# Kernel optimization log

Hardware: AMD Instinct MI355X
Metric: run time of the kernel (lower is better)

The kernel has to match this reference:

```python
import jax, jax.numpy as jnp
import numpy as np

NUM_GROUPS = 4194304  # 2^22 groups
GROUP_SIZE = 32
PACKED_GROUP_SIZE = GROUP_SIZE // 2 + 1  # 16 data bytes + 1 scale byte


def setup_inputs() -> dict:
    key = jax.random.key(0)
    packed = jax.random.randint(key, (NUM_GROUPS * PACKED_GROUP_SIZE,), 0, 256, dtype=jnp.int32)
    return {"packed": packed, "group_size": GROUP_SIZE, "ebits": 2, "mbits": 1}


def reference(packed, group_size, ebits, mbits):
    # MX4 -> fp32 dequantization: unpack 4-bit nibbles + per-group exp2 scale.
    packed_group_size = group_size // 2 + 1
    num_groups = packed.shape[0] // packed_group_size
    clamp_max = 2 ** (2 ** ebits - 1)                      # 8 for ebits=2
    max_val = clamp_max * (2.0 - 2.0 ** (-mbits))          # 12.0 for mbits=1

    pg = packed.reshape(num_groups, packed_group_size)
    # last byte of each group is the shared scale exponent (biased by 127)
    log_scale = jnp.clip(pg[:, -1].astype(jnp.float32) - 127.0, -126.0, 127.0)
    group_scale = jnp.exp2(log_scale)                      # (num_groups,)

    data = pg[:, : group_size // 2]                        # (num_groups, group_size//2)
    low = (data & 15).astype(jnp.float32)
    high = ((data >> 4) & 15).astype(jnp.float32)
    # interleave low/high nibbles: element order [low0, high0, low1, high1, ...]
    unpacked = jnp.stack([low, high], axis=-1).reshape(num_groups, group_size)
    unpacked = unpacked - jnp.float32(clamp_max)

    out = unpacked / jnp.float32(max_val) * group_scale[:, None]
    return out.reshape(-1).astype(jnp.float32)
```

## Files before the change

### kernel.cpp

```cpp
#include <hip/hip_runtime.h>


constexpr int kGroupSize = 32;
constexpr int kPGS = kGroupSize / 2 + 1;

__global__ __launch_bounds__(256) void dequant_mxfp4_kernel(
    const int* __restrict__ packed,
    const int* __restrict__ ebits_p,
    const int* __restrict__ mbits_p,
    float* __restrict__ out,
    int n_vec4)
{
    int tid = blockIdx.x * 256 + threadIdx.x;
    if (tid >= n_vec4) return;

    int ebits = ebits_p[0];
    int mbits = mbits_p[0];
    float clamp_max = (float)(1 << ((1 << ebits) - 1));
    float inv_max   = 1.0f / (clamp_max * (2.0f - exp2f((float)(-mbits))));

    int g  = tid >> 3;
    int b0 = (tid & 7) * 2;
    int base = g * kPGS;

    int w0 = packed[base + b0];
    int w1 = packed[base + b0 + 1];
    int s  = packed[base + kGroupSize / 2];

    int e = s - 127;
    e = min(max(e, -126), 127);
    float coef = ldexpf(1.0f, e) * inv_max;

    float4 r;
    r.x = ((float)(w0 & 15)        - clamp_max) * coef;
    r.y = ((float)((w0 >> 4) & 15) - clamp_max) * coef;
    r.z = ((float)(w1 & 15)        - clamp_max) * coef;
    r.w = ((float)((w1 >> 4) & 15) - clamp_max) * coef;

    reinterpret_cast<float4*>(out)[tid] = r;
}

extern "C" void kernel_launch(void* const* d_in, const int* in_sizes, int n_in,
                              void* d_out, int out_size, void* d_ws, size_t ws_size,
                              hipStream_t stream) {
    const int* packed  = (const int*)d_in[0];
    const int* ebits_p = (const int*)d_in[2];
    const int* mbits_p = (const int*)d_in[3];
    float* out = (float*)d_out;

    int n_vec4 = out_size / 4;
    int grid = (n_vec4 + 255) / 256;
    dequant_mxfp4_kernel<<<grid, 256, 0, stream>>>(packed, ebits_p, mbits_p, out, n_vec4);
}
```

Before: 690.6 us.

## Stage packed groups in LDS with vectorized loads, process 128 groups per block

Each block now cooperatively copies 128 packed groups into shared memory using 16-byte vector loads, then each thread dequantizes four float4 outputs from LDS. This replaces per-thread unaligned scalar global loads, including the redundant scale reads, with coalesced wide loads. It adds a block-wide barrier and shared-memory traffic. Scale computation is also folded into a single ldexpf.

```diff
diff --git a/kernel.cpp b/kernel.cpp
--- a/kernel.cpp
+++ b/kernel.cpp
@@ -1,43 +1,65 @@
 #include <hip/hip_runtime.h>
 
 
-constexpr int kGroupSize = 32;
-constexpr int kPGS = kGroupSize / 2 + 1;
+constexpr int kPGS = 17;
+constexpr int kGroupsPerBlock = 128;
+constexpr int kWordsPerBlock = kGroupsPerBlock * kPGS;
+constexpr int kVec4PerBlock  = kGroupsPerBlock * 8;
 
 __global__ __launch_bounds__(256) void dequant_mxfp4_kernel(
     const int* __restrict__ packed,
     const int* __restrict__ ebits_p,
     const int* __restrict__ mbits_p,
     float* __restrict__ out,
-    int n_vec4)
+    int num_groups)
 {
-    int tid = blockIdx.x * 256 + threadIdx.x;
-    if (tid >= n_vec4) return;
+    __shared__ int lds[kWordsPerBlock];
 
-    int ebits = ebits_p[0];
-    int mbits = mbits_p[0];
-    float clamp_max = (float)(1 << ((1 << ebits) - 1));
-    float inv_max   = 1.0f / (clamp_max * (2.0f - exp2f((float)(-mbits))));
+    const int block_g0 = blockIdx.x * kGroupsPerBlock;
+    const int groups_here = min(kGroupsPerBlock, num_groups - block_g0);
+    const int words = groups_here * kPGS;
+    const int* src = packed + (size_t)block_g0 * kPGS;
 
-    int g  = tid >> 3;
-    int b0 = (tid & 7) * 2;
-    int base = g * kPGS;
+    if (words == kWordsPerBlock) {
+        const int4* __restrict__ src4 = (const int4*)src;
+        int4* lds4 = (int4*)lds;
+        #pragma unroll
+        for (int i = threadIdx.x; i < kWordsPerBlock / 4; i += 256)
+            lds4[i] = src4[i];
+    } else {
+        for (int i = threadIdx.x; i < words; i += 256)
+            lds[i] = src[i];
+    }
+    __syncthreads();
 
-    int w0 = packed[base + b0];
-    int w1 = packed[base + b0 + 1];
-    int s  = packed[base + kGroupSize / 2];
+    const int ebits = ebits_p[0];
+    const int mbits = mbits_p[0];
+    const float clamp_max = (float)(1 << ((1 << ebits) - 1));
+    const float inv_max   = 1.0f / (clamp_max * (2.0f - exp2f((float)(-mbits))));
 
-    int e = s - 127;
-    e = min(max(e, -126), 127);
-    float coef = ldexpf(1.0f, e) * inv_max;
+    float4* __restrict__ dst = (float4*)out + (size_t)blockIdx.x * kVec4PerBlock;
+    const int nv = groups_here * 8;
 
-    float4 r;
-    r.x = ((float)(w0 & 15)        - clamp_max) * coef;
-    r.y = ((float)((w0 >> 4) & 15) - clamp_max) * coef;
-    r.z = ((float)(w1 & 15)        - clamp_max) * coef;
-    r.w = ((float)((w1 >> 4) & 15) - clamp_max) * coef;
+    #pragma unroll
+    for (int it = 0; it < 4; ++it) {
+        int v = it * 256 + (int)threadIdx.x;
+        if (v >= nv) break;
+        int g = v >> 3;
+        int j = (v & 7) * 2;
+        int w0 = lds[g * kPGS + j];
+        int w1 = lds[g * kPGS + j + 1];
+        int s  = lds[g * kPGS + 16];
 
-    reinterpret_cast<float4*>(out)[tid] = r;
+        int e = min(max(s - 127, -126), 127);
+        float coef = ldexpf(inv_max, e);
+
+        float4 r;
+        r.x = ((float)(w0 & 15)        - clamp_max) * coef;
+        r.y = ((float)((w0 >> 4) & 15) - clamp_max) * coef;
+        r.z = ((float)(w1 & 15)        - clamp_max) * coef;
+        r.w = ((float)((w1 >> 4) & 15) - clamp_max) * coef;
+        dst[v] = r;
+    }
 }
 
 extern "C" void kernel_launch(void* const* d_in, const int* in_sizes, int n_in,
@@ -48,7 +70,7 @@
     const int* mbits_p = (const int*)d_in[3];
     float* out = (float*)d_out;
 
-    int n_vec4 = out_size / 4;
-    int grid = (n_vec4 + 255) / 256;
-    dequant_mxfp4_kernel<<<grid, 256, 0, stream>>>(packed, ebits_p, mbits_p, out, n_vec4);
+    int num_groups = in_sizes[0] / kPGS;
+    int grid = (num_groups + kGroupsPerBlock - 1) / kGroupsPerBlock;
+    dequant_mxfp4_kernel<<<grid, 256, 0, stream>>>(packed, ebits_p, mbits_p, out, num_groups);
 }
```

Result: no change. 691.8 us (+0.2%).
